# Performance work log

Hardware: AMD Instinct MI355X
Metric: run time of the kernel (lower is better)

Reference implementation:

```python
import jax, jax.numpy as jnp
import numpy as np

SCALES = [4, 4, 4, 2, 2, 2, 1, 1, 1]
NB = 9
DN = ('NCHW', 'OIHW', 'NCHW')


def conv(x, w, b, stride=1):
    y = jax.lax.conv_general_dilated(x, w, (stride, stride), 'SAME', dimension_numbers=DN)
    return y + b[None, :, None, None]


def resize(x, h, w):
    B, C = x.shape[:2]
    return jax.image.resize(x, (B, C, h, w), method='bilinear')


def warp(img, flow):
    # Backward bilinear warp, border padding, align_corners=True grid_sample
    # (normalized-grid math reduces to pixel coord + flow).
    B, C, H, W = img.shape
    gx = jnp.arange(W, dtype=img.dtype)
    gy = jnp.arange(H, dtype=img.dtype)
    sx = jnp.clip(gx[None, None, :] + flow[:, 0], 0.0, W - 1.0)  # (B,H,W)
    sy = jnp.clip(gy[None, :, None] + flow[:, 1], 0.0, H - 1.0)
    x0 = jnp.floor(sx); y0 = jnp.floor(sy)
    x1 = jnp.minimum(x0 + 1.0, W - 1.0); y1 = jnp.minimum(y0 + 1.0, H - 1.0)
    wx = (sx - x0)[:, None]; wy = (sy - y0)[:, None]  # (B,1,H,W)
    x0i = x0.astype(jnp.int32); x1i = x1.astype(jnp.int32)
    y0i = y0.astype(jnp.int32); y1i = y1.astype(jnp.int32)
    flat = img.reshape(B, C, H * W)

    def gather(yi, xi):
        idx = (yi * W + xi).reshape(B, 1, H * W)
        return jnp.take_along_axis(flat, idx, axis=2).reshape(B, C, H, W)

    v00 = gather(y0i, x0i); v01 = gather(y0i, x1i)
    v10 = gather(y1i, x0i); v11 = gather(y1i, x1i)
    return (v00 * (1 - wx) * (1 - wy) + v01 * wx * (1 - wy)
            + v10 * (1 - wx) * wy + v11 * wx * wy)


def block_fwd(w0a, b0a, w0b, b0b, wcb, bcb, wlast, blast, x_in, flow, scale):
    # MVFB block: downsample by 1/scale, encode at 1/4 res, residual conv stack,
    # transpose-conv decode, upsample back, flow scaled by (scale*2).
    B, _, H, W = x_in.shape
    sh, sw = H // scale, W // scale
    if scale != 1:
        x_in = resize(x_in, sh, sw)
        flow = resize(flow, sh, sw) * (1.0 / scale)
    t = jnp.concatenate([x_in, flow], 1)               # (B,17,sh,sw)
    t = jax.nn.relu(conv(t, w0a, b0a, 2))              # (B,40,sh/2,sw/2)
    t = jax.nn.relu(conv(t, w0b, b0b, 2))              # (B,80,sh/4,sw/4)
    r = t
    for j in range(wcb.shape[0]):                      # 4 conv layers (fixed)
        r = jax.nn.relu(conv(r, wcb[j], bcb[j]))
    t = t + r
    tmp = jax.lax.conv_transpose(t, wlast, (2, 2), 'SAME', dimension_numbers=DN)
    tmp = tmp + blast[None, :, None, None]             # (B,5,sh/2,sw/2)
    tmp = resize(tmp, H, W)
    return tmp[:, :4] * (scale * 2.0), tmp[:, 4:5]


def setup_inputs() -> dict:
    key = jax.random.key(0)
    ks = jax.random.split(key, 8)
    B, H, W = 4, 256, 448
    C, C2, CIN, RF = 80, 40, 17, 32
    s = 0.05
    n = lambda k, shp: jax.random.normal(k, shp, jnp.float32) * s
    return {
        'x': jax.random.uniform(ks[0], (B, 6, H, W), jnp.float32),
        'wr': n(ks[1], (RF, 6, 3, 3)), 'br': jnp.zeros((RF,), jnp.float32),
        'wl': n(ks[2], (NB, RF)), 'bl': jnp.zeros((NB,), jnp.float32),
        'w0a': n(ks[3], (NB, C2, CIN, 3, 3)), 'b0a': jnp.zeros((NB, C2), jnp.float32),
        'w0b': n(ks[4], (NB, C, C2, 3, 3)), 'b0b': jnp.zeros((NB, C), jnp.float32),
        'wcb': n(ks[5], (NB, 4, C, C, 3, 3)), 'bcb': jnp.zeros((NB, 4, C), jnp.float32),
        'wlast': n(ks[6], (NB, 5, C, 4, 4)), 'blast': jnp.zeros((NB, 5), jnp.float32),
    }


def reference(x, wr, br, wl, bl, w0a, b0a, w0b, b0b, wcb, bcb, wlast, blast):
    B, _, H, W = x.shape
    img0, img1 = x[:, :3], x[:, 3:6]
    # Routing head: conv + relu + global avg pool + linear + sigmoid
    r = jax.nn.relu(conv(x[:, :6], wr, br)).mean(axis=(2, 3))     # (B,32)
    v = jax.nn.sigmoid(r @ wl.T + bl)                              # (B,9)
    v = v / (v.sum(1, keepdims=True) + 1e-6) * 4.5
    ref = jnp.round(jnp.clip(v, 0.0, 1.0))                         # RoundSTE fwd

    flow_feed = jnp.zeros((B, 4, H, W), x.dtype)
    mask_feed = jnp.zeros((B, 1, H, W), x.dtype)
    flow_sum = jnp.zeros_like(flow_feed)
    mask_sum = jnp.zeros_like(mask_feed)
    w0, w1 = img0, img1
    for i in range(NB):
        x_in = jnp.concatenate([img0, img1, w0, w1, mask_feed], 1)  # (B,13,H,W)
        fd, md = block_fwd(w0a[i], b0a[i], w0b[i], b0b[i], wcb[i], bcb[i],
                           wlast[i], blast[i], x_in, flow_feed, SCALES[i])
        g = ref[0, i]  # 0/1 gate from batch elem 0, as in the source
        # g in {0,1}: multiply-gating is exactly equivalent to the Python-level
        # skip (skipped blocks contribute zero delta; re-warping with unchanged
        # flow reproduces the same warped images).
        fd = fd * g; md = md * g
        flow_sum = flow_sum + fd; mask_sum = mask_sum + md
        flow_feed = flow_feed + fd; mask_feed = mask_feed + md
        w0 = warp(img0, flow_feed[:, :2])
        w1 = warp(img1, flow_feed[:, 2:4])
    wf0 = warp(img0, flow_sum[:, :2])
    wf1 = warp(img1, flow_sum[:, 2:4])
    m = jax.nn.sigmoid(mask_sum)
    return jnp.clip(wf0 * m + wf1 * (1.0 - m), 0.0, 1.0)
```

## Files before the change

### kernel.cpp

```cpp
#include <hip/hip_runtime.h>
#include <hip/hip_bf16.h>
#include <cmath>

#define BN 4
#define HF 256
#define WF 448
#define HWF (HF*WF)
#define GBLK 448

typedef __attribute__((ext_vector_type(8))) short short8v;
typedef __attribute__((ext_vector_type(4))) float float4v;

__device__ __forceinline__ float clampf(float v, float lo, float hi) {
    return fminf(fmaxf(v, lo), hi);
}
__device__ __forceinline__ float bf2f(ushort u) {
    unsigned v = ((unsigned)u) << 16;
    return __builtin_bit_cast(float, v);
}
__device__ __forceinline__ ushort f2bf(float f) {
    unsigned u = __builtin_bit_cast(unsigned, f);
    unsigned r = u + 0x7FFFu + ((u >> 16) & 1u);
    return (ushort)(r >> 16);
}
__device__ __forceinline__ uint packhl(float v) {
    unsigned u = __builtin_bit_cast(unsigned, v);
    ushort hi = (ushort)(u >> 16);
    ushort lo = f2bf(v - bf2f(hi));
    return ((uint)hi << 16) | lo;
}
__device__ __forceinline__ float unpackhl(uint u) {
    return bf2f((ushort)(u >> 16)) + bf2f((ushort)(u & 0xffffu));
}

__global__ void gate_conv_kernel(const float* __restrict__ x,
                                 const float* __restrict__ wr,
                                 const float* __restrict__ br,
                                 double* __restrict__ partial) {
    __shared__ float wsh[32*54];
    __shared__ float bsh[32];
    int tid = threadIdx.x;
    for (int i = tid; i < 32*54; i += 256) wsh[i] = wr[i];
    if (tid < 32) bsh[tid] = br[tid];
    __syncthreads();
    int p = blockIdx.x*256 + tid;
    int y = p / WF, xx = p % WF;
    float acc[32];
    #pragma unroll
    for (int co = 0; co < 32; ++co) acc[co] = bsh[co];
    for (int ci = 0; ci < 6; ++ci) {
        const float* ip = x + (size_t)ci*HWF;
        float v[9];
        #pragma unroll
        for (int ky = 0; ky < 3; ++ky) {
            int iy = y + ky - 1;
            #pragma unroll
            for (int kx = 0; kx < 3; ++kx) {
                int ix = xx + kx - 1;
                v[ky*3+kx] = ((unsigned)iy < HF && (unsigned)ix < WF) ? ip[iy*WF+ix] : 0.0f;
            }
        }
        #pragma unroll
        for (int co = 0; co < 32; ++co) {
            const float* wp = &wsh[co*54 + ci*9];
            #pragma unroll
            for (int t = 0; t < 9; ++t) acc[co] = fmaf(v[t], wp[t], acc[co]);
        }
    }
    __shared__ float red[4][32];
    int lane = tid & 63, wave = tid >> 6;
    #pragma unroll
    for (int co = 0; co < 32; ++co) {
        float s = fmaxf(acc[co], 0.0f);
        for (int off = 32; off > 0; off >>= 1) s += __shfl_down(s, off);
        if (lane == 0) red[wave][co] = s;
    }
    __syncthreads();
    if (tid < 32) {
        double s = (double)red[0][tid] + (double)red[1][tid]
                 + (double)red[2][tid] + (double)red[3][tid];
        partial[tid*GBLK + blockIdx.x] = s;
    }
}

__global__ void gate_fc_kernel(const double* __restrict__ partial,
                               const float* __restrict__ wl,
                               const float* __restrict__ bl,
                               float* __restrict__ g) {
    __shared__ double rm[32];
    __shared__ double v[9];
    int i = threadIdx.x;
    if (i < 32) {
        double s = 0.0;
        for (int k = 0; k < GBLK; ++k) s += partial[i*GBLK + k];
        rm[i] = s / (double)HWF;
    }
    __syncthreads();
    if (i < 9) {
        double t = (double)bl[i];
        for (int c = 0; c < 32; ++c) t += rm[c] * (double)wl[i*32+c];
        v[i] = 1.0 / (1.0 + exp(-t));
    }
    __syncthreads();
    if (i == 0) {
        double s = 0.0;
        for (int k = 0; k < 9; ++k) s += v[k];
        for (int k = 0; k < 9; ++k) {
            double vn = v[k] / (s + 1e-6) * 4.5;
            vn = vn < 0.0 ? 0.0 : (vn > 1.0 ? 1.0 : vn);
            g[k] = (float)rint(vn);
        }
    }
}

__global__ void wprep_kernel(const float* __restrict__ w, ushort* __restrict__ o,
                             int nconv, int Cout, int Cin, int CoP, int Kpad) {
    int idx = blockIdx.x*blockDim.x + threadIdx.x;
    int total = nconv*2*9*CoP*Kpad;
    if (idx >= total) return;
    int k   = idx % Kpad;
    int co  = (idx / Kpad) % CoP;
    int tap = (idx / (Kpad*CoP)) % 9;
    int pl  = (idx / (Kpad*CoP*9)) % 2;
    int cv  = idx / (Kpad*CoP*9*2);
    float v = 0.0f;
    if (co < Cout && k < Cin)
        v = w[(((size_t)cv*Cout + co)*Cin + k)*9 + tap];
    unsigned u = __builtin_bit_cast(unsigned, v);
    ushort hi = (ushort)(u >> 16);
    o[idx] = (pl == 0) ? hi : f2bf(v - bf2f(hi));
}

__global__ void init_kernel(const float* __restrict__ x,
                            float* __restrict__ flow, float* __restrict__ mask,
                            float* __restrict__ w0, float* __restrict__ w1) {
    int idx = blockIdx.x * blockDim.x + threadIdx.x;
    if (idx < BN*4*HWF) flow[idx] = 0.0f;
    if (idx < BN*HWF)   mask[idx] = 0.0f;
    if (idx < BN*3*HWF) {
        int b = idx / (3*HWF), r = idx % (3*HWF);
        w0[idx] = x[(size_t)b*6*HWF + r];
        w1[idx] = x[(size_t)b*6*HWF + 3*HWF + r];
    }
}

__global__ void prepare1_kernel(const float* __restrict__ x,
                                const float* __restrict__ w0buf, const float* __restrict__ w1buf,
                                const float* __restrict__ mask, const float* __restrict__ flow,
                                const float* __restrict__ g, int gi,
                                uint* __restrict__ t) {
    if (g[gi] == 0.0f) return;
    const int SW1 = WF+1, SH1 = HF+1;
    int idx = blockIdx.x * blockDim.x + threadIdx.x;
    int total = BN*SH1*SW1;
    if (idx >= total) return;
    int ox = idx % SW1;
    int oy = (idx/SW1) % SH1;
    int b  = idx/(SW1*SH1);
    uint* dst = t + (size_t)idx*17;
    if (ox == WF || oy == HF) {
        #pragma unroll
        for (int c = 0; c < 17; ++c) dst[c] = 0u;
        return;
    }
    int p = oy*WF + ox;
    const float* xb = x + (size_t)b*6*HWF;
    #pragma unroll
    for (int c = 0; c < 6; ++c)  dst[c]    = packhl(xb[(size_t)c*HWF + p]);
    #pragma unroll
    for (int c = 0; c < 3; ++c)  dst[6+c]  = packhl(w0buf[((size_t)b*3 + c)*HWF + p]);
    #pragma unroll
    for (int c = 0; c < 3; ++c)  dst[9+c]  = packhl(w1buf[((size_t)b*3 + c)*HWF + p]);
    dst[12] = packhl(mask[(size_t)b*HWF + p]);
    #pragma unroll
    for (int c = 0; c < 4; ++c)  dst[13+c] = packhl(flow[((size_t)b*4 + c)*HWF + p]);
}

__global__ void prep_h_kernel(const float* __restrict__ x,
                              const float* __restrict__ w0buf, const float* __restrict__ w1buf,
                              const float* __restrict__ mask, const float* __restrict__ flow,
                              const float* __restrict__ g, int gi,
                              float* __restrict__ inter, int s, int sw) {
    if (g[gi] == 0.0f) return;
    int idx = blockIdx.x*blockDim.x + threadIdx.x;
    int total = 17*BN*HF*sw;
    if (idx >= total) return;
    int ox = idx % sw;
    int y  = (idx/sw) % HF;
    int b  = (idx/(sw*HF)) % BN;
    int c  = idx/(sw*HF*BN);
    const float* src; float mult = 1.0f;
    if (c < 6)        src = x + ((size_t)b*6 + c)*HWF;
    else if (c < 9)   src = w0buf + ((size_t)b*3 + (c-6))*HWF;
    else if (c < 12)  src = w1buf + ((size_t)b*3 + (c-9))*HWF;
    else if (c == 12) src = mask + (size_t)b*HWF;
    else { src = flow + ((size_t)b*4 + (c-13))*HWF; mult = 1.0f/(float)s; }
    int nt = 2*s;
    float posx = (ox + 0.5f)*(float)s - 0.5f;
    int jx0 = s*ox - s/2;
    const float* rp = src + (size_t)y*WF;
    float acc = 0.f, sx = 0.f;
    for (int k = 0; k < nt; ++k) {
        int j = jx0 + k;
        float ww = 1.0f - fabsf((float)j - posx)/(float)s;
        if (j < 0 || j >= WF) ww = 0.f;
        sx += ww;
        if (ww != 0.f) acc += ww * rp[j];
    }
    inter[idx] = acc * mult / sx;
}

__global__ void prep_v_kernel(const float* __restrict__ inter,
                              const float* __restrict__ g, int gi,
                              uint* __restrict__ t, int s, int sh, int sw) {
    if (g[gi] == 0.0f) return;
    int SW1 = sw+1, SH1 = sh+1;
    int idx = blockIdx.x*blockDim.x + threadIdx.x;
    int total = BN*SH1*SW1*4;
    if (idx >= total) return;
    int cg  = idx & 3;
    int pix = idx >> 2;
    int ox = pix % SW1;
    int oy = (pix/SW1) % SH1;
    int b  = pix/(SW1*SH1);
    const int startA[4] = {0,5,9,13};
    const int cntA[4]   = {5,4,4,4};
    int cs = startA[cg], cn = cntA[cg];
    uint* dst = t + (size_t)pix*17 + cs;
    if (ox == sw || oy == sh) {
        for (int c = 0; c < cn; ++c) dst[c] = 0u;
        return;
    }
    int nt = 2*s;
    float posy = (oy + 0.5f)*(float)s - 0.5f;
    int jy0 = s*oy - s/2;
    float wy[8]; float sy = 0.f;
    for (int k = 0; k < nt; ++k) {
        int j = jy0 + k;
        float ww = 1.0f - fabsf((float)j - posy)/(float)s;
        if (j < 0 || j >= HF) ww = 0.f;
        wy[k] = ww; sy += ww;
    }
    float inv = 1.0f / sy;
    for (int c = 0; c < cn; ++c) {
        const float* ip = inter + ((size_t)((cs+c)*BN + b)*HF)*sw + ox;
        float acc = 0.f;
        for (int k = 0; k < nt; ++k) {
            if (wy[k] != 0.f) acc += wy[k] * ip[(size_t)(jy0 + k)*sw];
        }
        dst[c] = packhl(acc * inv);
    }
}

__global__ void haloz_kernel(uint* __restrict__ t0, uint* __restrict__ t1,
                             uint* __restrict__ ra, uint* __restrict__ rb,
                             const float* __restrict__ g, int gi,
                             int h, int w, int h2, int w2) {
    if (g[gi] == 0.0f) return;
    int W1 = w+1, H1 = h+1;
    int idx = blockIdx.x*blockDim.x + threadIdx.x;
    if (idx >= BN*H1*W1) return;
    int px = idx % (H1*W1);
    int b  = idx / (H1*W1);
    int x = px % W1, y = px / W1;
    if (y == h || x == w) {
        uint* p = t0 + ((size_t)b*H1*W1 + px)*40;
        for (int c = 0; c < 40; ++c) p[c] = 0u;
    }
    int W2 = w2+2, H2 = h2+2;
    if (y < H2 && x < W2 && (y == 0 || y == H2-1 || x == 0 || x == W2-1)) {
        size_t o = ((size_t)b*H2*W2 + (size_t)y*W2 + x)*80;
        for (int c = 0; c < 80; ++c) { t1[o+c] = 0u; ra[o+c] = 0u; rb[o+c] = 0u; }
    }
}

template<int S, int CIN, int COUT, int SPLIT>
__global__ __launch_bounds__(64)
void conv_pk_kernel(const uint* __restrict__ in, int inWP, size_t inBS,
                    const ushort* __restrict__ wt,
                    const float* __restrict__ bias,
                    const uint* __restrict__ resid,
                    const float* __restrict__ g, int gi,
                    uint* __restrict__ out, int outWP, size_t outBS,
                    int Hout, int Wout) {
    if (g[gi] == 0.0f) return;
    constexpr int KPAD  = ((CIN + 31)/32)*32;
    constexpr int KC    = KPAD/32;
    constexpr int COP   = (SPLIT == 2) ? 96 : 48;
    constexpr int NSTEP = KC*9;
    constexpr int PADO  = (S == 1) ? 1 : 0;
    constexpr size_t LOFF = (size_t)9*COP*KPAD;

    int ntx = (Wout + 15)/16;
    int nty = Hout/2;
    int bx  = blockIdx.x % ntx;
    int t2  = blockIdx.x / ntx;
    int by  = t2 % nty; t2 /= nty;
    int half = t2 % SPLIT;
    int b    = t2 / SPLIT;
    int coB  = half*40;

    int lane = threadIdx.x;
    int l15 = lane & 15, l4 = lane >> 4;
    int ox  = bx*16 + l15;
    int oy0 = by*2;

    float4v acc[2][3];
    #pragma unroll
    for (int n = 0; n < 2; ++n)
        #pragma unroll
        for (int m = 0; m < 3; ++m)
            acc[n][m] = (float4v){0.f,0.f,0.f,0.f};

    const uint* inb = in + (size_t)b*inBS;
    const uint* bbase[2];
    #pragma unroll
    for (int n = 0; n < 2; ++n) {
        int iy = (oy0 + n)*S - PADO;
        int ix = ox*S - PADO;
        bbase[n] = inb + ((size_t)iy*inWP + ix)*CIN + l4*8;
    }
    const ushort* wbase = wt + ((size_t)(coB + l15))*KPAD + l4*8;

    short8v whA[3][3], wlA[3][3];
    uint bu[3][2][8];

    auto ISSUE = [&](int s) {
        int tap = s % 9, kc = s / 9;
        int dy = tap/3, dx = tap%3;
        int slot = s % 3;
        #pragma unroll
        for (int n = 0; n < 2; ++n) {
            const uint* p = bbase[n] + ((size_t)dy*inWP + dx)*CIN + kc*32;
            __builtin_memcpy(&bu[slot][n][0], p, 32);
        }
        #pragma unroll
        for (int m = 0; m < 3; ++m) {
            const ushort* wp = wbase + (size_t)(tap*COP + m*16)*KPAD + kc*32;
            whA[slot][m] = *(const short8v*)wp;
            wlA[slot][m] = *(const short8v*)(wp + LOFF);
        }
    };
    auto COMPUTE = [&](int s) {
        int slot = s % 3;
        short8v bhi[2], blo[2];
        #pragma unroll
        for (int n = 0; n < 2; ++n)
            #pragma unroll
            for (int j = 0; j < 8; ++j) {
                bhi[n][j] = (short)(bu[slot][n][j] >> 16);
                blo[n][j] = (short)(bu[slot][n][j] & 0xffffu);
            }
        #pragma unroll
        for (int m = 0; m < 3; ++m)
            #pragma unroll
            for (int n = 0; n < 2; ++n) {
                acc[n][m] = __builtin_amdgcn_mfma_f32_16x16x32_bf16(whA[slot][m], bhi[n], acc[n][m], 0, 0, 0);
                acc[n][m] = __builtin_amdgcn_mfma_f32_16x16x32_bf16(whA[slot][m], blo[n], acc[n][m], 0, 0, 0);
                acc[n][m] = __builtin_amdgcn_mfma_f32_16x16x32_bf16(wlA[slot][m], bhi[n], acc[n][m], 0, 0, 0);
            }
    };

    ISSUE(0);
    if (NSTEP > 1) ISSUE(1);
    if (NSTEP > 2) ISSUE(2);
    #pragma unroll
    for (int s = 0; s < NSTEP; ++s) {
        COMPUTE(s);
        if (s + 3 < NSTEP) ISSUE(s + 3);
    }

    if (ox < Wout) {
        #pragma unroll
        for (int n = 0; n < 2; ++n) {
            int oy = oy0 + n;
            size_t pbase = (size_t)b*outBS + ((size_t)oy*outWP + ox)*COUT + coB;
            #pragma unroll
            for (int m = 0; m < 3; ++m)
                #pragma unroll
                for (int r = 0; r < 4; ++r) {
                    int rel = m*16 + l4*4 + r;
                    if (rel < 40) {
                        float v = fmaxf(acc[n][m][r] + bias[coB + rel], 0.0f);
                        if (resid) v += unpackhl(resid[pbase + rel]);
                        out[pbase + rel] = packhl(v);
                    }
                }
        }
    }
}

__global__ void deconv_kernel(const uint* __restrict__ t, int WP, size_t BS,
                              const float* __restrict__ wl,
                              const float* __restrict__ bl,
                              const float* __restrict__ g, int gi,
                              float* __restrict__ out,
                              int h2, int w2) {
    if (g[gi] == 0.0f) return;
    int ho = 2*h2, wo = 2*w2;
    int idx = blockIdx.x * blockDim.x + threadIdx.x;
    int total = BN*5*ho*wo;
    if (idx >= total) return;
    int xx = idx % wo;
    int y  = (idx / wo) % ho;
    int o  = (idx / (wo*ho)) % 5;
    int b  = idx / (wo*ho*5);
    float acc = bl[o];
    int p = y & 1, q = xx & 1;
    const uint* tb = t + (size_t)b*BS;
    for (int dy = 0; dy < 2; ++dy) {
        int ky = p + 2*dy;
        int iy = (y + ky - 2) >> 1;
        if ((unsigned)iy >= (unsigned)h2) continue;
        for (int dx = 0; dx < 2; ++dx) {
            int kx = q + 2*dx;
            int ix = (xx + kx - 2) >> 1;
            if ((unsigned)ix >= (unsigned)w2) continue;
            const uint* tp = tb + ((size_t)iy*WP + ix)*80;
            const float* wp = wl + (size_t)o*80*16 + ky*4 + kx;
            for (int i = 0; i < 80; ++i)
                acc += unpackhl(tp[i]) * wp[i*16];
        }
    }
    out[idx] = acc;
}

__global__ void upwarp_kernel(const float* __restrict__ tmp,
                              const float* __restrict__ x,
                              const float* __restrict__ g, int gi,
                              float* __restrict__ flow, float* __restrict__ mask,
                              float* __restrict__ w0, float* __restrict__ w1,
                              int h, int w, int f, float fdscale) {
    float gg = g[gi];
    if (gg == 0.0f) return;
    int idx = blockIdx.x * blockDim.x + threadIdx.x;
    if (idx >= BN*HWF) return;
    int p2 = idx % HWF;
    int b  = idx / HWF;
    int xx = p2 % WF, y = p2 / WF;

    float posy = (y + 0.5f)/(float)f - 0.5f;
    float posx = (xx + 0.5f)/(float)f - 0.5f;
    float y0f = floorf(posy), x0f = floorf(posx);
    int jy0 = (int)y0f, jx0 = (int)x0f;
    float fy = posy - y0f, fx = posx - x0f;
    int jy1 = min(jy0 + 1, h-1), jx1 = min(jx0 + 1, w-1);
    jy0 = max(jy0, 0); jx0 = max(jx0, 0);
    float w00 = (1-fx)*(1-fy), w01 = fx*(1-fy), w10 = (1-fx)*fy, w11 = fx*fy;

    float fl[4];
    #pragma unroll
    for (int c = 0; c < 4; ++c) {
        const float* tp = tmp + ((size_t)(b*5 + c))*h*w;
        float val = tp[jy0*w+jx0]*w00 + tp[jy0*w+jx1]*w01 + tp[jy1*w+jx0]*w10 + tp[jy1*w+jx1]*w11;
        size_t fo = ((size_t)b*4 + c)*HWF + p2;
        float nf = flow[fo] + val * fdscale * gg;
        flow[fo] = nf;
        fl[c] = nf;
    }
    {
        const float* tp = tmp + ((size_t)(b*5 + 4))*h*w;
        float val = tp[jy0*w+jx0]*w00 + tp[jy0*w+jx1]*w01 + tp[jy1*w+jx0]*w10 + tp[jy1*w+jx1]*w11;
        mask[(size_t)b*HWF + p2] += val * gg;
    }

    #pragma unroll
    for (int which = 0; which < 2; ++which) {
        float sx = clampf((float)xx + fl[which*2+0], 0.f, (float)(WF-1));
        float sy = clampf((float)y  + fl[which*2+1], 0.f, (float)(HF-1));
        float sx0f = floorf(sx), sy0f = floorf(sy);
        int ix0 = (int)sx0f, iy0 = (int)sy0f;
        int ix1 = min(ix0 + 1, WF - 1), iy1 = min(iy0 + 1, HF - 1);
        float wx = sx - sx0f, wy = sy - sy0f;
        float a00 = (1-wx)*(1-wy), a01 = wx*(1-wy), a10 = (1-wx)*wy, a11 = wx*wy;
        float* dst = which ? w1 : w0;
        #pragma unroll
        for (int c = 0; c < 3; ++c) {
            const float* im = x + ((size_t)b*6 + which*3 + c)*HWF;
            float val = im[iy0*WF+ix0]*a00 + im[iy0*WF+ix1]*a01
                      + im[iy1*WF+ix0]*a10 + im[iy1*WF+ix1]*a11;
            dst[((size_t)b*3 + c)*HWF + p2] = val;
        }
    }
}

__global__ void final_kernel(const float* __restrict__ w0, const float* __restrict__ w1,
                             const float* __restrict__ mask, float* __restrict__ outp) {
    int idx = blockIdx.x*blockDim.x + threadIdx.x;
    if (idx >= BN*3*HWF) return;
    int p = idx % HWF;
    int b = idx / (3*HWF);
    float m = 1.0f / (1.0f + expf(-mask[(size_t)b*HWF + p]));
    float val = w0[idx]*m + w1[idx]*(1.0f - m);
    outp[idx] = clampf(val, 0.0f, 1.0f);
}

extern "C" void kernel_launch(void* const* d_in, const int* in_sizes, int n_in,
                              void* d_out, int out_size, void* d_ws, size_t ws_size,
                              hipStream_t stream) {
    const float* x     = (const float*)d_in[0];
    const float* wr    = (const float*)d_in[1];
    const float* br    = (const float*)d_in[2];
    const float* wl    = (const float*)d_in[3];
    const float* bl    = (const float*)d_in[4];
    const float* w0a   = (const float*)d_in[5];
    const float* b0a   = (const float*)d_in[6];
    const float* w0b   = (const float*)d_in[7];
    const float* b0b   = (const float*)d_in[8];
    const float* wcb   = (const float*)d_in[9];
    const float* bcb   = (const float*)d_in[10];
    const float* wlast = (const float*)d_in[11];
    const float* blast = (const float*)d_in[12];

    float* ws       = (float*)d_ws;
    double* partial = (double*)d_ws;
    float* g        = ws + 28672;
    size_t off = 28688;
    float* flow = ws + off; off += (size_t)BN*4*HWF;
    float* mask = ws + off; off += (size_t)BN*1*HWF;
    float* wb0  = ws + off; off += (size_t)BN*3*HWF;
    float* wb1  = ws + off; off += (size_t)BN*3*HWF;
    uint*  tinr = (uint*)(ws + off); off += 7900000;
    uint*  t0   = (uint*)(ws + off); off += 4644000;
    float* tmpb = ws + off; off += (size_t)BN*5*(HF/2)*(WF/2);
    ushort* wTa2 = (ushort*)(ws + off); off += (size_t)9*2*9*48*32/2;
    ushort* wTb2 = (ushort*)(ws + off); off += (size_t)9*2*9*96*64/2;
    ushort* wTc2 = (ushort*)(ws + off); off += (size_t)36*2*9*96*96/2;
    uint* t1 = tinr;
    uint* ra = tinr + 2407680;
    uint* rb = tinr + 4815360;
    float* inter = (float*)t0;

    gate_conv_kernel<<<GBLK, 256, 0, stream>>>(x, wr, br, partial);
    gate_fc_kernel<<<1, 64, 0, stream>>>(partial, wl, bl, g);
    {
        int n = 9*2*9*48*32;
        wprep_kernel<<<(n+255)/256, 256, 0, stream>>>(w0a, wTa2, 9, 40, 17, 48, 32);
        n = 9*2*9*96*64;
        wprep_kernel<<<(n+255)/256, 256, 0, stream>>>(w0b, wTb2, 9, 80, 40, 96, 64);
        n = 36*2*9*96*96;
        wprep_kernel<<<(n+255)/256, 256, 0, stream>>>(wcb, wTc2, 36, 80, 80, 96, 96);
    }
    {
        int n = BN*4*HWF;
        init_kernel<<<(n+255)/256, 256, 0, stream>>>(x, flow, mask, wb0, wb1);
    }
    const int SC[9] = {4,4,4,2,2,2,1,1,1};
    for (int i = 0; i < 9; ++i) {
        int s = SC[i];
        int sh = HF/s, sw = WF/s;
        int h = sh/2, w = sw/2;
        int h2 = h/2, w2 = w/2;
        int tinWP = sw+1;             size_t tinBS = (size_t)(sh+1)*(sw+1)*17;
        int t0WP  = w+1;              size_t t0BS  = (size_t)(h+1)*(w+1)*40;
        int t1WP  = w2+2;             size_t t1BS  = (size_t)(h2+2)*(w2+2)*80;
        size_t ioff = ((size_t)t1WP + 1)*80;
        if (s == 1) {
            int n = BN*(sh+1)*(sw+1);
            prepare1_kernel<<<(n+255)/256,256,0,stream>>>(x, wb0, wb1, mask, flow, g, i, tinr);
        } else {
            int n1 = 17*BN*HF*sw;
            prep_h_kernel<<<(n1+255)/256,256,0,stream>>>(x, wb0, wb1, mask, flow, g, i, inter, s, sw);
            int n2 = BN*(sh+1)*(sw+1)*4;
            prep_v_kernel<<<(n2+255)/256,256,0,stream>>>(inter, g, i, tinr, s, sh, sw);
        }
        {
            int ntx = (w + 15)/16;
            int nblk = ntx*(h/2)*1*BN;
            conv_pk_kernel<2,17,40,1><<<nblk, 64, 0, stream>>>(
                tinr, tinWP, tinBS, wTa2 + (size_t)i*2*9*48*32, b0a + i*40, nullptr,
                g, i, t0, t0WP, t0BS, h, w);
        }
        {
            int n = BN*(h+1)*(w+1);
            haloz_kernel<<<(n+255)/256,256,0,stream>>>(t0, t1, ra, rb, g, i, h, w, h2, w2);
        }
        {
            int ntx = (w2 + 15)/16;
            int nblk = ntx*(h2/2)*2*BN;
            conv_pk_kernel<2,40,80,2><<<nblk, 64, 0, stream>>>(
                t0, t0WP, t0BS, wTb2 + (size_t)i*2*9*96*64, b0b + i*80, nullptr,
                g, i, t1 + ioff, t1WP, t1BS, h2, w2);
        }
        {
            int ntx = (w2 + 15)/16;
            int nblk = ntx*(h2/2)*2*BN;
            const uint* cin = t1 + ioff;
            uint* couts[4] = {ra, rb, ra, rb};
            for (int j = 0; j < 4; ++j) {
                const uint* res = (j == 3) ? (t1 + ioff) : nullptr;
                conv_pk_kernel<1,80,80,2><<<nblk, 64, 0, stream>>>(
                    cin, t1WP, t1BS, wTc2 + ((size_t)i*4 + j)*2*9*96*96, bcb + ((size_t)i*4 + j)*80,
                    res, g, i, couts[j] + ioff, t1WP, t1BS, h2, w2);
                cin = couts[j] + ioff;
            }
        }
        {
            int n = BN*5*h*w;
            deconv_kernel<<<(n+255)/256,256,0,stream>>>(rb + ioff, t1WP, t1BS,
                wlast + (size_t)i*5*80*16, blast + i*5, g, i, tmpb, h2, w2);
        }
        {
            int n = BN*HWF;
            upwarp_kernel<<<(n+255)/256,256,0,stream>>>(tmpb, x, g, i, flow, mask, wb0, wb1,
                h, w, 2*s, (float)(2*s));
        }
    }
    {
        int n = BN*3*HWF;
        final_kernel<<<(n+255)/256,256,0,stream>>>(wb0, wb1, mask, (float*)d_out);
    }
}
```

Before: 1.369 ms.

## Fuse full-res input packing and final blend into upwarp, retune conv row tiling

Measured after the change: 1.239 ms, median of 2. 1.1x faster.

```diff
diff --git a/kernel.cpp b/kernel.cpp
--- a/kernel.cpp
+++ b/kernel.cpp
@@ -113,11 +113,8 @@
     }
 }
 
-__global__ void wprep_kernel(const float* __restrict__ w, ushort* __restrict__ o,
-                             int nconv, int Cout, int Cin, int CoP, int Kpad) {
-    int idx = blockIdx.x*blockDim.x + threadIdx.x;
-    int total = nconv*2*9*CoP*Kpad;
-    if (idx >= total) return;
+__device__ __forceinline__ void wprep_one(const float* __restrict__ w, ushort* __restrict__ o,
+                                          int idx, int Cout, int Cin, int CoP, int Kpad) {
     int k   = idx % Kpad;
     int co  = (idx / Kpad) % CoP;
     int tap = (idx / (Kpad*CoP)) % 9;
@@ -130,6 +127,18 @@
     ushort hi = (ushort)(u >> 16);
     o[idx] = (pl == 0) ? hi : f2bf(v - bf2f(hi));
 }
+__global__ void wprep_all_kernel(const float* __restrict__ w0a, const float* __restrict__ w0b,
+                                 const float* __restrict__ wcb,
+                                 ushort* __restrict__ a, ushort* __restrict__ b,
+                                 ushort* __restrict__ c) {
+    const int NA = 9*2*9*48*32;
+    const int NB = 9*2*9*96*64;
+    const int NC = 36*2*9*96*96;
+    int idx = blockIdx.x*blockDim.x + threadIdx.x;
+    if (idx < NA) wprep_one(w0a, a, idx, 40, 17, 48, 32);
+    else if (idx < NA+NB) wprep_one(w0b, b, idx-NA, 80, 40, 96, 64);
+    else if (idx < NA+NB+NC) wprep_one(wcb, c, idx-NA-NB, 80, 80, 96, 96);
+}
 
 __global__ void init_kernel(const float* __restrict__ x,
                             float* __restrict__ flow, float* __restrict__ mask,
@@ -142,38 +151,6 @@
         w0[idx] = x[(size_t)b*6*HWF + r];
         w1[idx] = x[(size_t)b*6*HWF + 3*HWF + r];
     }
-}
-
-__global__ void prepare1_kernel(const float* __restrict__ x,
-                                const float* __restrict__ w0buf, const float* __restrict__ w1buf,
-                                const float* __restrict__ mask, const float* __restrict__ flow,
-                                const float* __restrict__ g, int gi,
-                                uint* __restrict__ t) {
-    if (g[gi] == 0.0f) return;
-    const int SW1 = WF+1, SH1 = HF+1;
-    int idx = blockIdx.x * blockDim.x + threadIdx.x;
-    int total = BN*SH1*SW1;
-    if (idx >= total) return;
-    int ox = idx % SW1;
-    int oy = (idx/SW1) % SH1;
-    int b  = idx/(SW1*SH1);
-    uint* dst = t + (size_t)idx*17;
-    if (ox == WF || oy == HF) {
-        #pragma unroll
-        for (int c = 0; c < 17; ++c) dst[c] = 0u;
-        return;
-    }
-    int p = oy*WF + ox;
-    const float* xb = x + (size_t)b*6*HWF;
-    #pragma unroll
-    for (int c = 0; c < 6; ++c)  dst[c]    = packhl(xb[(size_t)c*HWF + p]);
-    #pragma unroll
-    for (int c = 0; c < 3; ++c)  dst[6+c]  = packhl(w0buf[((size_t)b*3 + c)*HWF + p]);
-    #pragma unroll
-    for (int c = 0; c < 3; ++c)  dst[9+c]  = packhl(w1buf[((size_t)b*3 + c)*HWF + p]);
-    dst[12] = packhl(mask[(size_t)b*HWF + p]);
-    #pragma unroll
-    for (int c = 0; c < 4; ++c)  dst[13+c] = packhl(flow[((size_t)b*4 + c)*HWF + p]);
 }
 
 __global__ void prep_h_kernel(const float* __restrict__ x,
@@ -274,7 +251,7 @@
     }
 }
 
-template<int S, int CIN, int COUT, int SPLIT>
+template<int S, int CIN, int COUT, int SPLIT, int R>
 __global__ __launch_bounds__(64)
 void conv_pk_kernel(const uint* __restrict__ in, int inWP, size_t inBS,
                     const ushort* __restrict__ wt,
@@ -292,7 +269,7 @@
     constexpr size_t LOFF = (size_t)9*COP*KPAD;
 
     int ntx = (Wout + 15)/16;
-    int nty = Hout/2;
+    int nty = Hout/R;
     int bx  = blockIdx.x % ntx;
     int t2  = blockIdx.x / ntx;
     int by  = t2 % nty; t2 /= nty;
@@ -303,19 +280,19 @@
     int lane = threadIdx.x;
     int l15 = lane & 15, l4 = lane >> 4;
     int ox  = bx*16 + l15;
-    int oy0 = by*2;
-
-    float4v acc[2][3];
+    int oy0 = by*R;
+
+    float4v acc[R][3];
     #pragma unroll
-    for (int n = 0; n < 2; ++n)
+    for (int n = 0; n < R; ++n)
         #pragma unroll
         for (int m = 0; m < 3; ++m)
             acc[n][m] = (float4v){0.f,0.f,0.f,0.f};
 
     const uint* inb = in + (size_t)b*inBS;
-    const uint* bbase[2];
+    const uint* bbase[R];
     #pragma unroll
-    for (int n = 0; n < 2; ++n) {
+    for (int n = 0; n < R; ++n) {
         int iy = (oy0 + n)*S - PADO;
         int ix = ox*S - PADO;
         bbase[n] = inb + ((size_t)iy*inWP + ix)*CIN + l4*8;
@@ -323,14 +300,14 @@
     const ushort* wbase = wt + ((size_t)(coB + l15))*KPAD + l4*8;
 
     short8v whA[3][3], wlA[3][3];
-    uint bu[3][2][8];
+    uint bu[3][R][8];
 
     auto ISSUE = [&](int s) {
         int tap = s % 9, kc = s / 9;
         int dy = tap/3, dx = tap%3;
         int slot = s % 3;
         #pragma unroll
-        for (int n = 0; n < 2; ++n) {
+        for (int n = 0; n < R; ++n) {
             const uint* p = bbase[n] + ((size_t)dy*inWP + dx)*CIN + kc*32;
             __builtin_memcpy(&bu[slot][n][0], p, 32);
         }
@@ -343,9 +320,9 @@
     };
     auto COMPUTE = [&](int s) {
         int slot = s % 3;
-        short8v bhi[2], blo[2];
-        #pragma unroll
-        for (int n = 0; n < 2; ++n)
+        short8v bhi[R], blo[R];
+        #pragma unroll
+        for (int n = 0; n < R; ++n)
             #pragma unroll
             for (int j = 0; j < 8; ++j) {
                 bhi[n][j] = (short)(bu[slot][n][j] >> 16);
@@ -354,7 +331,7 @@
         #pragma unroll
         for (int m = 0; m < 3; ++m)
             #pragma unroll
-            for (int n = 0; n < 2; ++n) {
+            for (int n = 0; n < R; ++n) {
                 acc[n][m] = __builtin_amdgcn_mfma_f32_16x16x32_bf16(whA[slot][m], bhi[n], acc[n][m], 0, 0, 0);
                 acc[n][m] = __builtin_amdgcn_mfma_f32_16x16x32_bf16(whA[slot][m], blo[n], acc[n][m], 0, 0, 0);
                 acc[n][m] = __builtin_amdgcn_mfma_f32_16x16x32_bf16(wlA[slot][m], bhi[n], acc[n][m], 0, 0, 0);
@@ -372,7 +349,7 @@
 
     if (ox < Wout) {
         #pragma unroll
-        for (int n = 0; n < 2; ++n) {
+        for (int n = 0; n < R; ++n) {
             int oy = oy0 + n;
             size_t pbase = (size_t)b*outBS + ((size_t)oy*outWP + ox)*COUT + coB;
             #pragma unroll
@@ -425,16 +402,26 @@
     out[idx] = acc;
 }
 
+template<int MODE>
 __global__ void upwarp_kernel(const float* __restrict__ tmp,
                               const float* __restrict__ x,
                               const float* __restrict__ g, int gi,
                               float* __restrict__ flow, float* __restrict__ mask,
                               float* __restrict__ w0, float* __restrict__ w1,
+                              uint* __restrict__ tin, float* __restrict__ outp,
                               int h, int w, int f, float fdscale) {
     float gg = g[gi];
-    if (gg == 0.0f) return;
+    if (MODE == 0 && gg == 0.0f) return;
     int idx = blockIdx.x * blockDim.x + threadIdx.x;
     if (idx >= BN*HWF) return;
+    if (MODE == 1 && idx < BN*705) {
+        int b = idx / 705, k = idx % 705;
+        int hy, hx;
+        if (k < 449) { hy = 256; hx = k; } else { hy = k - 449; hx = 448; }
+        uint* hd = tin + (((size_t)b*257 + hy)*449 + hx)*17;
+        #pragma unroll
+        for (int c = 0; c < 17; ++c) hd[c] = 0u;
+    }
     int p2 = idx % HWF;
     int b  = idx / HWF;
     int xx = p2 % WF, y = p2 / WF;
@@ -455,15 +442,18 @@
         float val = tp[jy0*w+jx0]*w00 + tp[jy0*w+jx1]*w01 + tp[jy1*w+jx0]*w10 + tp[jy1*w+jx1]*w11;
         size_t fo = ((size_t)b*4 + c)*HWF + p2;
         float nf = flow[fo] + val * fdscale * gg;
-        flow[fo] = nf;
+        if (MODE != 2) flow[fo] = nf;
         fl[c] = nf;
     }
+    float nm;
     {
         const float* tp = tmp + ((size_t)(b*5 + 4))*h*w;
         float val = tp[jy0*w+jx0]*w00 + tp[jy0*w+jx1]*w01 + tp[jy1*w+jx0]*w10 + tp[jy1*w+jx1]*w11;
-        mask[(size_t)b*HWF + p2] += val * gg;
-    }
-
+        nm = mask[(size_t)b*HWF + p2] + val * gg;
+        if (MODE != 2) mask[(size_t)b*HWF + p2] = nm;
+    }
+
+    float wv[2][3];
     #pragma unroll
     for (int which = 0; which < 2; ++which) {
         float sx = clampf((float)xx + fl[which*2+0], 0.f, (float)(WF-1));
@@ -473,26 +463,40 @@
         int ix1 = min(ix0 + 1, WF - 1), iy1 = min(iy0 + 1, HF - 1);
         float wx = sx - sx0f, wy = sy - sy0f;
         float a00 = (1-wx)*(1-wy), a01 = wx*(1-wy), a10 = (1-wx)*wy, a11 = wx*wy;
-        float* dst = which ? w1 : w0;
         #pragma unroll
         for (int c = 0; c < 3; ++c) {
             const float* im = x + ((size_t)b*6 + which*3 + c)*HWF;
-            float val = im[iy0*WF+ix0]*a00 + im[iy0*WF+ix1]*a01
-                      + im[iy1*WF+ix0]*a10 + im[iy1*WF+ix1]*a11;
-            dst[((size_t)b*3 + c)*HWF + p2] = val;
-        }
-    }
-}
-
-__global__ void final_kernel(const float* __restrict__ w0, const float* __restrict__ w1,
-                             const float* __restrict__ mask, float* __restrict__ outp) {
-    int idx = blockIdx.x*blockDim.x + threadIdx.x;
-    if (idx >= BN*3*HWF) return;
-    int p = idx % HWF;
-    int b = idx / (3*HWF);
-    float m = 1.0f / (1.0f + expf(-mask[(size_t)b*HWF + p]));
-    float val = w0[idx]*m + w1[idx]*(1.0f - m);
-    outp[idx] = clampf(val, 0.0f, 1.0f);
+            wv[which][c] = im[iy0*WF+ix0]*a00 + im[iy0*WF+ix1]*a01
+                         + im[iy1*WF+ix0]*a10 + im[iy1*WF+ix1]*a11;
+        }
+    }
+
+    if (MODE == 0) {
+        #pragma unroll
+        for (int c = 0; c < 3; ++c) {
+            w0[((size_t)b*3 + c)*HWF + p2] = wv[0][c];
+            w1[((size_t)b*3 + c)*HWF + p2] = wv[1][c];
+        }
+    } else if (MODE == 1) {
+        uint* dst = tin + (((size_t)b*257 + y)*449 + xx)*17;
+        const float* xb = x + (size_t)b*6*HWF;
+        #pragma unroll
+        for (int c = 0; c < 6; ++c) dst[c] = packhl(xb[(size_t)c*HWF + p2]);
+        #pragma unroll
+        for (int c = 0; c < 3; ++c) dst[6+c] = packhl(wv[0][c]);
+        #pragma unroll
+        for (int c = 0; c < 3; ++c) dst[9+c] = packhl(wv[1][c]);
+        dst[12] = packhl(nm);
+        #pragma unroll
+        for (int c = 0; c < 4; ++c) dst[13+c] = packhl(fl[c]);
+    } else {
+        float m = 1.0f / (1.0f + expf(-nm));
+        #pragma unroll
+        for (int c = 0; c < 3; ++c) {
+            float val = wv[0][c]*m + wv[1][c]*(1.0f - m);
+            outp[((size_t)b*3 + c)*HWF + p2] = clampf(val, 0.0f, 1.0f);
+        }
+    }
 }
 
 extern "C" void kernel_launch(void* const* d_in, const int* in_sizes, int n_in,
@@ -534,12 +538,8 @@
     gate_conv_kernel<<<GBLK, 256, 0, stream>>>(x, wr, br, partial);
     gate_fc_kernel<<<1, 64, 0, stream>>>(partial, wl, bl, g);
     {
-        int n = 9*2*9*48*32;
-        wprep_kernel<<<(n+255)/256, 256, 0, stream>>>(w0a, wTa2, 9, 40, 17, 48, 32);
-        n = 9*2*9*96*64;
-        wprep_kernel<<<(n+255)/256, 256, 0, stream>>>(w0b, wTb2, 9, 80, 40, 96, 64);
-        n = 36*2*9*96*96;
-        wprep_kernel<<<(n+255)/256, 256, 0, stream>>>(wcb, wTc2, 36, 80, 80, 96, 96);
+        int n = 9*2*9*48*32 + 9*2*9*96*64 + 36*2*9*96*96;
+        wprep_all_kernel<<<(n+255)/256, 256, 0, stream>>>(w0a, w0b, wcb, wTa2, wTb2, wTc2);
     }
     {
         int n = BN*4*HWF;
@@ -555,10 +555,7 @@
         int t0WP  = w+1;              size_t t0BS  = (size_t)(h+1)*(w+1)*40;
         int t1WP  = w2+2;             size_t t1BS  = (size_t)(h2+2)*(w2+2)*80;
         size_t ioff = ((size_t)t1WP + 1)*80;
-        if (s == 1) {
-            int n = BN*(sh+1)*(sw+1);
-            prepare1_kernel<<<(n+255)/256,256,0,stream>>>(x, wb0, wb1, mask, flow, g, i, tinr);
-        } else {
+        if (s > 1) {
             int n1 = 17*BN*HF*sw;
             prep_h_kernel<<<(n1+255)/256,256,0,stream>>>(x, wb0, wb1, mask, flow, g, i, inter, s, sw);
             int n2 = BN*(sh+1)*(sw+1)*4;
@@ -566,10 +563,15 @@
         }
         {
             int ntx = (w + 15)/16;
-            int nblk = ntx*(h/2)*1*BN;
-            conv_pk_kernel<2,17,40,1><<<nblk, 64, 0, stream>>>(
-                tinr, tinWP, tinBS, wTa2 + (size_t)i*2*9*48*32, b0a + i*40, nullptr,
-                g, i, t0, t0WP, t0BS, h, w);
+            if (h >= 128) {
+                conv_pk_kernel<2,17,40,1,2><<<ntx*(h/2)*BN, 64, 0, stream>>>(
+                    tinr, tinWP, tinBS, wTa2 + (size_t)i*2*9*48*32, b0a + i*40, nullptr,
+                    g, i, t0, t0WP, t0BS, h, w);
+            } else {
+                conv_pk_kernel<2,17,40,1,1><<<ntx*h*BN, 64, 0, stream>>>(
+                    tinr, tinWP, tinBS, wTa2 + (size_t)i*2*9*48*32, b0a + i*40, nullptr,
+                    g, i, t0, t0WP, t0BS, h, w);
+            }
         }
         {
             int n = BN*(h+1)*(w+1);
@@ -577,19 +579,18 @@
         }
         {
             int ntx = (w2 + 15)/16;
-            int nblk = ntx*(h2/2)*2*BN;
-            conv_pk_kernel<2,40,80,2><<<nblk, 64, 0, stream>>>(
+            conv_pk_kernel<2,40,80,2,1><<<ntx*h2*2*BN, 64, 0, stream>>>(
                 t0, t0WP, t0BS, wTb2 + (size_t)i*2*9*96*64, b0b + i*80, nullptr,
                 g, i, t1 + ioff, t1WP, t1BS, h2, w2);
         }
         {
             int ntx = (w2 + 15)/16;
-            int nblk = ntx*(h2/2)*2*BN;
+            int nblk = ntx*h2*2*BN;
             const uint* cin = t1 + ioff;
             uint* couts[4] = {ra, rb, ra, rb};
             for (int j = 0; j < 4; ++j) {
                 const uint* res = (j == 3) ? (t1 + ioff) : nullptr;
-                conv_pk_kernel<1,80,80,2><<<nblk, 64, 0, stream>>>(
+                conv_pk_kernel<1,80,80,2,1><<<nblk, 64, 0, stream>>>(
                     cin, t1WP, t1BS, wTc2 + ((size_t)i*4 + j)*2*9*96*96, bcb + ((size_t)i*4 + j)*80,
                     res, g, i, couts[j] + ioff, t1WP, t1BS, h2, w2);
                 cin = couts[j] + ioff;
@@ -602,12 +603,16 @@
         }
         {
             int n = BN*HWF;
-            upwarp_kernel<<<(n+255)/256,256,0,stream>>>(tmpb, x, g, i, flow, mask, wb0, wb1,
-                h, w, 2*s, (float)(2*s));
-        }
-    }
-    {
-        int n = BN*3*HWF;
-        final_kernel<<<(n+255)/256,256,0,stream>>>(wb0, wb1, mask, (float*)d_out);
-    }
-}
+            int nb = (n+255)/256;
+            if (i < 5)
+                upwarp_kernel<0><<<nb,256,0,stream>>>(tmpb, x, g, i, flow, mask, wb0, wb1,
+                    nullptr, nullptr, h, w, 2*s, (float)(2*s));
+            else if (i < 8)
+                upwarp_kernel<1><<<nb,256,0,stream>>>(tmpb, x, g, i, flow, mask, wb0, wb1,
+                    tinr, nullptr, h, w, 2*s, (float)(2*s));
+            else
+                upwarp_kernel<2><<<nb,256,0,stream>>>(tmpb, x, g, i, flow, mask, wb0, wb1,
+                    nullptr, (float*)d_out, h, w, 2*s, (float)(2*s));
+        }
+    }
+}
```
